# Performance work log

Measured on AMD Instinct MI355X. Metric: run time of the kernel, lower is better.

## Reference

```python
import jax, jax.numpy as jnp
import numpy as np

B, S, D, H = 2, 2048, 2048, 16
DH = D // H  # 128


def _rope_tables(seq_len, head_dim, base=10000.0):
    inv_freq = 1.0 / (base ** (jnp.arange(0, head_dim, 2, dtype=jnp.float32) / head_dim))
    t = jnp.arange(seq_len, dtype=jnp.float32)
    freqs = jnp.outer(t, inv_freq)                      # [S, DH/2]
    emb = jnp.concatenate([freqs, freqs], axis=-1)      # [S, DH]
    return jnp.cos(emb), jnp.sin(emb)


def _rotate_half(x):
    x1, x2 = jnp.split(x, 2, axis=-1)
    return jnp.concatenate([-x2, x1], axis=-1)


def setup_inputs() -> dict:
    key = jax.random.key(0)
    ks = jax.random.split(key, 5)
    sc = 0.02
    return {
        "hidden_states": jax.random.normal(ks[0], (B, S, D), jnp.float32),
        "Wq": jax.random.normal(ks[1], (D, D), jnp.float32) * sc,
        "Wk": jax.random.normal(ks[2], (D, D), jnp.float32) * sc,
        "Wv": jax.random.normal(ks[3], (D, D), jnp.float32) * sc,
        "Wo": jax.random.normal(ks[4], (D, D), jnp.float32) * sc,
        "medical_bias": jnp.zeros((1, H, 1, 1), jnp.float32),
    }


def reference(hidden_states, Wq, Wk, Wv, Wo, medical_bias):
    b, s, _ = hidden_states.shape
    # torch Linear: y = x @ W.T  (W is [out, in])
    def proj(x, W):
        y = jnp.einsum('bsd,ed->bse', x, W)
        return y.reshape(b, s, H, DH).transpose(0, 2, 1, 3)  # [b,H,s,DH]

    q = proj(hidden_states, Wq)
    k = proj(hidden_states, Wk)
    v = proj(hidden_states, Wv)

    cos, sin = _rope_tables(s, DH)                 # [s, DH]
    cos = cos[None, None]                          # [1,1,s,DH]
    sin = sin[None, None]
    q = q * cos + _rotate_half(q) * sin
    k = k * cos + _rotate_half(k) * sin

    scores = jnp.einsum('bhqd,bhkd->bhqk', q, k) / jnp.sqrt(jnp.float32(DH))
    scores = scores + medical_bias                 # learned per-head bias
    probs = jax.nn.softmax(scores, axis=-1)
    out = jnp.einsum('bhqk,bhkd->bhqd', probs, v)  # [b,H,s,DH]
    out = out.transpose(0, 2, 1, 3).reshape(b, s, D)
    return jnp.einsum('bsd,ed->bse', out, Wo)
```

## Files before the change

kernel.cpp:

```cpp
#include <hip/hip_runtime.h>
#include <hip/hip_bf16.h>
#include <stdint.h>


#define B_ 2
#define S_ 2048
#define D_ 2048
#define H_ 16

typedef float f32x4 __attribute__((ext_vector_type(4)));
typedef short s16x8 __attribute__((ext_vector_type(8)));

__device__ __forceinline__ unsigned short f2bf(float f) {
  union { float f; uint32_t u; } c; c.f = f;
  return (unsigned short)((c.u + 0x7fffu + ((c.u >> 16) & 1u)) >> 16);
}

__device__ __forceinline__ unsigned short bfc(float f) {
  __hip_bfloat16 h = __float2bfloat16(f);
  unsigned short u;
  __builtin_memcpy(&u, &h, 2);
  return u;
}

#define FAST_EXP2(x) __builtin_amdgcn_exp2f(x)

__device__ __forceinline__ void gld_lds16(const void* g, void* l) {
  __builtin_amdgcn_global_load_lds(
      (const __attribute__((address_space(1))) uint32_t*)g,
      (__attribute__((address_space(3))) uint32_t*)l, 16, 0, 0);
}

__global__ __launch_bounds__(256) void k_f2bf_all(
    const float* __restrict__ hs, const float* __restrict__ wq,
    const float* __restrict__ wk, const float* __restrict__ wv,
    const float* __restrict__ wo, unsigned short* __restrict__ hb,
    unsigned short* __restrict__ wall, float2* __restrict__ t2) {
  const int NH = 2097152, NW = 1048576;
  const int NF = NH + 4 * NW;
  const int NT = 131072;
  int i = blockIdx.x * 256 + threadIdx.x;
  const int stride = gridDim.x * 256;
  for (; i < NF + NT; i += stride) {
    if (i < NF) {
      f32x4 v;
      ushort4* dst;
      if (i < NH) {
        v = ((const f32x4*)hs)[i];
        dst = (ushort4*)hb + i;
      } else {
        const int j = i - NH;
        const int rgn = j >> 20;
        const int o = j & (NW - 1);
        const float* s = (rgn == 0) ? wq : (rgn == 1) ? wk : (rgn == 2) ? wv : wo;
        v = ((const f32x4*)s)[o];
        dst = (ushort4*)wall + j;
      }
      ushort4 u;
      u.x = f2bf(v.x); u.y = f2bf(v.y); u.z = f2bf(v.z); u.w = f2bf(v.w);
      *dst = u;
    } else {
      const int t = i - NF;
      const int s = t >> 6, j = t & 63;
      float inv = expf(-(float)j * (1.0f / 64.0f) * 9.210340371976184f);
      float sv, cv;
      sincosf((float)s * inv, &sv, &cv);
      t2[t] = float2{cv, sv};
    }
  }
}

__global__ __launch_bounds__(256, 2) void k_gemm(
    const unsigned short* __restrict__ A,
    const unsigned short* __restrict__ W0,
    const unsigned short* __restrict__ W1,
    const unsigned short* __restrict__ W2,
    float* __restrict__ C0,
    unsigned short* __restrict__ Qo,
    unsigned short* __restrict__ Ko,
    unsigned short* __restrict__ VT,
    const float2* __restrict__ tab,
    int plain) {
  __shared__ unsigned short Al[2][128 * 64];
  __shared__ unsigned short Bl[2][128 * 64];

  const int l0 = ((int)blockIdx.z * 32 + (int)blockIdx.y) * 16 + (int)blockIdx.x;
  const int qx = ((int)gridDim.z * 512) >> 3;
  const int wg = (l0 & 7) * qx + (l0 >> 3);
  const int z = wg >> 9;
  const unsigned short* __restrict__ Wp = (z == 0) ? W0 : (z == 1) ? W1 : W2;

  const int tid = threadIdx.x;
  const int w = tid >> 6;
  const int l = tid & 63;
  const int row0 = ((wg >> 4) & 31) * 128;
  const int col0 = (wg & 15) * 128;

  const int c16 = l & 15, g = l >> 4;
  const int cx = c16 & 7;

  const int srow = l >> 3;
  const int sslot = (l & 7) ^ (l >> 3);
  const int scol = sslot << 3;

  int kbase[2];
#pragma unroll
  for (int kk = 0; kk < 2; ++kk)
    kbase[kk] = c16 * 128 + (((kk * 4 + g) ^ cx) << 4);
  const char* AW0 = (const char*)&Al[0][0] + w * 4096;
  const char* AW1 = (const char*)&Al[1][0] + w * 4096;
  const char* BB0 = (const char*)&Bl[0][0];
  const char* BB1 = (const char*)&Bl[1][0];

  f32x4 acc[2][8];
#pragma unroll
  for (int m = 0; m < 2; ++m)
#pragma unroll
    for (int n = 0; n < 8; ++n)
      acc[m][n] = f32x4{0.f, 0.f, 0.f, 0.f};

#define STAGE_G(K0, BUF)                                                       \
  do {                                                                         \
    _Pragma("unroll") for (int i = 0; i < 4; ++i) {                            \
      const int jj = (w << 2) + i;                                             \
      gld_lds16(&A[(size_t)(row0 + (jj << 3) + srow) * 2048 + (K0) + scol],    \
                &Al[BUF][jj * 512]);                                           \
      gld_lds16(&Wp[(size_t)(col0 + (jj << 3) + srow) * 2048 + (K0) + scol],   \
                &Bl[BUF][jj * 512]);                                           \
    }                                                                          \
  } while (0)

#define COMPUTE_G(AW, BBp)                                                     \
  do {                                                                         \
    _Pragma("unroll") for (int kk = 0; kk < 2; ++kk) {                         \
      s16x8 a[2], b[8];                                                        \
      _Pragma("unroll") for (int m = 0; m < 2; ++m)                            \
          a[m] = *(const s16x8*)((AW) + m * 2048 + kbase[kk]);                 \
      _Pragma("unroll") for (int n = 0; n < 8; ++n)                            \
          b[n] = *(const s16x8*)((BBp) + n * 2048 + kbase[kk]);                \
      __builtin_amdgcn_s_setprio(1);                                           \
      _Pragma("unroll") for (int m = 0; m < 2; ++m)                            \
          _Pragma("unroll") for (int n = 0; n < 8; ++n)                        \
              acc[m][n] = __builtin_amdgcn_mfma_f32_16x16x32_bf16(             \
                  a[m], b[n], acc[m][n], 0, 0, 0);                             \
      __builtin_amdgcn_s_setprio(0);                                           \
    }                                                                          \
  } while (0)

  STAGE_G(0, 0);
  __syncthreads();
  for (int k0 = 0; k0 < 2048; k0 += 128) {
    STAGE_G(k0 + 64, 1);
    COMPUTE_G(AW0, BB0);
    __syncthreads();
    if (k0 + 128 < 2048) STAGE_G(k0 + 128, 0);
    COMPUTE_G(AW1, BB1);
    __syncthreads();
  }
#undef STAGE_G
#undef COMPUTE_G

  if (plain) {
#pragma unroll
    for (int m = 0; m < 2; ++m) {
      const int gr = row0 + w * 32 + m * 16 + g * 4;
#pragma unroll
      for (int n = 0; n < 8; ++n) {
        const int gc = col0 + n * 16 + c16;
#pragma unroll
        for (int r = 0; r < 4; ++r)
          C0[(size_t)(gr + r) * 2048 + gc] = acc[m][n][r];
      }
    }
  } else if (z == 2) {
#pragma unroll
    for (int m = 0; m < 2; ++m) {
      const int gr = row0 + w * 32 + m * 16 + g * 4;
      const int b_ = gr >> 11, s_ = gr & 2047;
#pragma unroll
      for (int n = 0; n < 8; ++n) {
        const int gc = col0 + n * 16 + c16;
        ushort4 o;
        o.x = f2bf(acc[m][n][0]);
        o.y = f2bf(acc[m][n][1]);
        o.z = f2bf(acc[m][n][2]);
        o.w = f2bf(acc[m][n][3]);
        *(ushort4*)&VT[((size_t)(b_ * 2048 + gc)) * 2048 + s_] = o;
      }
    }
  } else {
    unsigned short* __restrict__ O = z ? Ko : Qo;
    const float sc = z ? 1.0f : (0.08838834764831845f * 1.4426950408889634f);
#pragma unroll
    for (int m = 0; m < 2; ++m) {
#pragma unroll
      for (int r = 0; r < 4; ++r) {
        const int gr = row0 + w * 32 + m * 16 + g * 4 + r;
        const int s_ = gr & 2047;
#pragma unroll
        for (int n = 0; n < 4; ++n) {
          const float2 f = tab[s_ * 64 + n * 16 + c16];
          const float x1 = acc[m][n][r], x2 = acc[m][n + 4][r];
          O[(size_t)gr * 2048 + col0 + n * 16 + c16] =
              f2bf((x1 * f.x - x2 * f.y) * sc);
          O[(size_t)gr * 2048 + col0 + 64 + n * 16 + c16] =
              f2bf((x2 * f.x + x1 * f.y) * sc);
        }
      }
    }
  }
}

__global__ __launch_bounds__(256, 2) void k_attn(
    const unsigned short* __restrict__ Qb,
    const unsigned short* __restrict__ Kb,
    const unsigned short* __restrict__ Vt,
    unsigned short* __restrict__ Ob) {
  __shared__ unsigned short Kl[2][64 * 128];
  __shared__ unsigned short Vl[2][128 * 64];
  __shared__ unsigned short Pl[4][16 * 64];

  const int l0 = (int)blockIdx.y * 16 + (int)blockIdx.x;
  const int wg = (l0 & 7) * 64 + (l0 >> 3);
  const int bh = wg >> 4;
  const int b = bh >> 4, h = bh & 15;

  const int tid = threadIdx.x, w = tid >> 6, l = tid & 63;
  const int q0 = (wg & 15) * 128 + w * 32;
  const int g = l >> 4, c16 = l & 15;
  const int cx = c16 & 7;

  int kaddr[4], vaddr[2];
#pragma unroll
  for (int kc = 0; kc < 4; ++kc)
    kaddr[kc] = c16 * 256 + ((((kc * 4 + g) ^ cx)) << 4);
#pragma unroll
  for (int kc2 = 0; kc2 < 2; ++kc2)
    vaddr[kc2] = c16 * 128 + ((((kc2 * 4 + g) ^ cx)) << 4);
  const char* PW = (const char*)&Pl[w][0];

  s16x8 qf[2][4];
#pragma unroll
  for (int qq = 0; qq < 2; ++qq)
#pragma unroll
    for (int kc = 0; kc < 4; ++kc)
      qf[qq][kc] = *(const s16x8*)&Qb[(size_t)(b * 2048 + q0 + qq * 16 + c16) * 2048 +
                                      h * 128 + kc * 32 + g * 8];

  f32x4 oacc[2][8];
  float mrow[2][4], lrow[2][4];
#pragma unroll
  for (int qq = 0; qq < 2; ++qq) {
#pragma unroll
    for (int df = 0; df < 8; ++df) oacc[qq][df] = f32x4{0.f, 0.f, 0.f, 0.f};
#pragma unroll
    for (int r = 0; r < 4; ++r) { mrow[qq][r] = -INFINITY; lrow[qq][r] = 0.f; }
  }

#define STAGE(T, BUF)                                                          \
  do {                                                                         \
    _Pragma("unroll") for (int i = 0; i < 4; ++i) {                            \
      const int jj = (w << 2) + i;                                             \
      const int krow = jj * 4 + (l >> 4);                                      \
      const int kslot = (l & 15) ^ (krow & 7);                                 \
      gld_lds16(&Kb[(size_t)(b * 2048 + (T) + krow) * 2048 + h * 128 +        \
                    (kslot << 3)],                                             \
                &Kl[BUF][jj * 512]);                                           \
      const int vrow = jj * 8 + (l >> 3);                                      \
      const int vslot = (l & 7) ^ (vrow & 7);                                  \
      gld_lds16(&Vt[(size_t)(bh * 128 + vrow) * 2048 + (T) + (vslot << 3)],    \
                &Vl[BUF][jj * 512]);                                           \
    }                                                                          \
  } while (0)

#define COMPUTE(BUF_)                                                          \
  do {                                                                         \
    f32x4 sacc[2][4];                                                          \
    _Pragma("unroll") for (int qq = 0; qq < 2; ++qq)                           \
        _Pragma("unroll") for (int n = 0; n < 4; ++n)                          \
            sacc[qq][n] = f32x4{0.f, 0.f, 0.f, 0.f};                           \
    const char* KB = (const char*)&Kl[BUF_][0];                                \
    __builtin_amdgcn_s_setprio(1);                                             \
    _Pragma("unroll") for (int kc = 0; kc < 4; ++kc) {                         \
      s16x8 kb[4];                                                             \
      _Pragma("unroll") for (int n = 0; n < 4; ++n)                            \
          kb[n] = *(const s16x8*)(KB + kaddr[kc] + n * 4096);                  \
      _Pragma("unroll") for (int qq = 0; qq < 2; ++qq)                         \
          _Pragma("unroll") for (int n = 0; n < 4; ++n)                        \
              sacc[qq][n] = __builtin_amdgcn_mfma_f32_16x16x32_bf16(           \
                  qf[qq][kc], kb[n], sacc[qq][n], 0, 0, 0);                    \
    }                                                                          \
    __builtin_amdgcn_s_setprio(0);                                             \
            \
    float mx4[2][4];                                                           \
    float need = 0.f;                                                          \
    _Pragma("unroll") for (int qq = 0; qq < 2; ++qq)                           \
        _Pragma("unroll") for (int r = 0; r < 4; ++r) {                        \
      mx4[qq][r] = fmaxf(fmaxf(sacc[qq][0][r], sacc[qq][1][r]),                \
                         fmaxf(sacc[qq][2][r], sacc[qq][3][r]));               \
      need = fmaxf(need, mx4[qq][r] - mrow[qq][r]);                            \
    }                                                                          \
    if (!__all(need <= 8.0f)) {          \
      _Pragma("unroll") for (int qq = 0; qq < 2; ++qq)                         \
          _Pragma("unroll") for (int r = 0; r < 4; ++r) {                      \
        float mx = mx4[qq][r];                                                 \
        mx = fmaxf(mx, __shfl_xor(mx, 1));                                     \
        mx = fmaxf(mx, __shfl_xor(mx, 2));                                     \
        mx = fmaxf(mx, __shfl_xor(mx, 4));                                     \
        mx = fmaxf(mx, __shfl_xor(mx, 8));                                     \
        float mnew = fmaxf(mrow[qq][r], mx);                                   \
        float alpha = FAST_EXP2(mrow[qq][r] - mnew);                           \
        mrow[qq][r] = mnew;                                                    \
        lrow[qq][r] *= alpha;                                                  \
        _Pragma("unroll") for (int df = 0; df < 8; ++df)                       \
            oacc[qq][df][r] *= alpha;                                          \
      }                                                                        \
    }                                                                          \
    const char* VB = (const char*)&Vl[BUF_][0];                                \
       \
      \
    _Pragma("unroll") for (int qq = 0; qq < 2; ++qq) {                         \
      _Pragma("unroll") for (int r = 0; r < 4; ++r) {                          \
        float rs = 0.f;                                                        \
        _Pragma("unroll") for (int n = 0; n < 4; ++n) {                        \
          float p = FAST_EXP2(sacc[qq][n][r] - mrow[qq][r]);                   \
          sacc[qq][n][r] = p;                                                  \
          rs += p;                                                             \
        }                                                                      \
        lrow[qq][r] += rs;                                                     \
      }                                                                        \
      _Pragma("unroll") for (int n = 0; n < 4; ++n)                            \
          _Pragma("unroll") for (int r = 0; r < 4; ++r) {                      \
        const int prow = g * 4 + r;                                            \
        const int psl = (n * 2 + (c16 >> 3)) ^ (prow & 7);                     \
        Pl[w][prow * 64 + (psl << 3) + (c16 & 7)] = bfc(sacc[qq][n][r]);       \
      }                                                                        \
      __builtin_amdgcn_s_setprio(1);                                           \
      _Pragma("unroll") for (int kc2 = 0; kc2 < 2; ++kc2) {                    \
        s16x8 pa = *(const s16x8*)(PW + vaddr[kc2]);                           \
        _Pragma("unroll") for (int df = 0; df < 8; ++df) {                     \
          s16x8 vb = *(const s16x8*)(VB + vaddr[kc2] + df * 2048);             \
          oacc[qq][df] = __builtin_amdgcn_mfma_f32_16x16x32_bf16(              \
              pa, vb, oacc[qq][df], 0, 0, 0);                                  \
        }                                                                      \
      }                                                                        \
      __builtin_amdgcn_s_setprio(0);                                           \
    }                                                                          \
  } while (0)

  STAGE(0, 0);
  __syncthreads();
  for (int t = 0; t < 2048; t += 128) {
    STAGE(t + 64, 1);
    COMPUTE(0);
    __syncthreads();
    if (t + 128 < 2048) STAGE(t + 128, 0);
    COMPUTE(1);
    __syncthreads();
  }
#undef STAGE
#undef COMPUTE

#pragma unroll
  for (int qq = 0; qq < 2; ++qq)
#pragma unroll
    for (int r = 0; r < 4; ++r) {
      float tot = lrow[qq][r];
      tot += __shfl_xor(tot, 1);
      tot += __shfl_xor(tot, 2);
      tot += __shfl_xor(tot, 4);
      tot += __shfl_xor(tot, 8);
      const float inv = 1.0f / tot;
      const int srow_ = q0 + qq * 16 + g * 4 + r;
#pragma unroll
      for (int df = 0; df < 8; ++df)
        Ob[(size_t)(b * 2048 + srow_) * 2048 + h * 128 + df * 16 + c16] =
            bfc(oacc[qq][df][r] * inv);
    }
}

extern "C" void kernel_launch(void* const* d_in, const int* in_sizes, int n_in,
                              void* d_out, int out_size, void* d_ws, size_t ws_size,
                              hipStream_t stream) {
  const float* hs = (const float*)d_in[0];
  const float* Wq = (const float*)d_in[1];
  const float* Wk = (const float*)d_in[2];
  const float* Wv = (const float*)d_in[3];
  const float* Wo = (const float*)d_in[4];
  float* out = (float*)d_out;
  char* ws = (char*)d_ws;

  unsigned short* hb   = (unsigned short*)(ws + 0);
  unsigned short* wall = (unsigned short*)(ws + 16777216);
  unsigned short* wqb  = wall;
  unsigned short* wkb  = wall + 4194304;
  unsigned short* wvb  = wall + 8388608;
  unsigned short* wob  = wall + 12582912;
  unsigned short* Qbb  = (unsigned short*)(ws + 50331648);
  unsigned short* Kbb  = (unsigned short*)(ws + 67108864);
  unsigned short* Vt   = (unsigned short*)(ws + 83886080);
  float2*         tab2 = (float2*)(ws + 100663296);
  unsigned short* Ob   = hb;

  k_f2bf_all<<<2048, 256, 0, stream>>>(hs, Wq, Wk, Wv, Wo, hb, wall, tab2);

  k_gemm<<<dim3(16, 32, 3), 256, 0, stream>>>(hb, wqb, wkb, wvb, nullptr, Qbb,
                                              Kbb, Vt, tab2, 0);
  k_attn<<<dim3(16, 32), 256, 0, stream>>>(Qbb, Kbb, Vt, Ob);
  k_gemm<<<dim3(16, 32, 1), 256, 0, stream>>>(Ob, wob, nullptr, nullptr, out,
                                              nullptr, nullptr, nullptr, tab2, 1);
}
```

Baseline: 254.1 us.

## Use 256x256 tiles with 512 threads for fused QKV projection GEMM

Adds a dedicated QKV GEMM kernel with 256x256 output tiles, 8 waves, and 128KB of LDS double buffering. Loads are synchronised with explicit vmcnt waits and raw barriers, which gives more operand reuse per loaded byte than the 128x128 tiles. The RoPE epilogue now stages accumulators through LDS so each thread writes coalesced rows. The output projection keeps the original kernel with the mode branches removed. Occupancy drops to one large block per CU, and the grid shrinks to 384 blocks, which may cause tail or load-balance effects.

```diff
diff --git a/kernel.cpp b/kernel.cpp
--- a/kernel.cpp
+++ b/kernel.cpp
@@ -70,25 +70,164 @@
   }
 }
 
-__global__ __launch_bounds__(256, 2) void k_gemm(
+__global__ __launch_bounds__(512, 1) void k_gemm3(
     const unsigned short* __restrict__ A,
     const unsigned short* __restrict__ W0,
     const unsigned short* __restrict__ W1,
     const unsigned short* __restrict__ W2,
-    float* __restrict__ C0,
     unsigned short* __restrict__ Qo,
     unsigned short* __restrict__ Ko,
     unsigned short* __restrict__ VT,
-    const float2* __restrict__ tab,
-    int plain) {
+    const float2* __restrict__ tab) {
+  __shared__ unsigned short Sm[65536];
+
+  const int l0 = ((int)blockIdx.z * 16 + (int)blockIdx.y) * 8 + (int)blockIdx.x;
+  const int wg = (l0 & 7) * 48 + (l0 >> 3);
+  const int z = wg >> 7;
+  const int ww = wg & 127;
+  const int row0 = (ww >> 3) * 256;
+  const int col0 = (ww & 7) * 256;
+  const unsigned short* __restrict__ Wp = (z == 0) ? W0 : (z == 1) ? W1 : W2;
+
+  const int tid = threadIdx.x;
+  const int w = tid >> 6, l = tid & 63;
+  const int wr = w >> 2, wc = w & 3;
+  const int c16 = l & 15, g = l >> 4;
+  const int cx = c16 & 7;
+
+  const int srow = w * 8 + (l >> 3);
+  int kbase[2];
+#pragma unroll
+  for (int kk = 0; kk < 2; ++kk)
+    kbase[kk] = c16 * 128 + (((kk * 4 + g) ^ cx) << 4);
+
+  char* smb = (char*)Sm;
+  const char* AB0 = smb + wr * 16384;
+  const char* AB1 = smb + 32768 + wr * 16384;
+  const char* BB0 = smb + 65536 + wc * 8192;
+  const char* BB1 = smb + 98304 + wc * 8192;
+
+  f32x4 acc[8][4];
+#pragma unroll
+  for (int m = 0; m < 8; ++m)
+#pragma unroll
+    for (int n = 0; n < 4; ++n)
+      acc[m][n] = f32x4{0.f, 0.f, 0.f, 0.f};
+
+#define STAGE3(K0, BUF)                                                        \
+  do {                                                                         \
+    _Pragma("unroll") for (int i = 0; i < 4; ++i) {                            \
+      const int rr = i * 64 + srow;                                            \
+      const int sl = (l & 7) ^ (rr & 7);                                       \
+      gld_lds16(&A[(size_t)(row0 + rr) * 2048 + (K0) + sl * 8],                \
+                Sm + (BUF)*16384 + (i * 64 + w * 8) * 64);                     \
+      gld_lds16(&Wp[(size_t)(col0 + rr) * 2048 + (K0) + sl * 8],               \
+                Sm + 32768 + (BUF)*16384 + (i * 64 + w * 8) * 64);             \
+    }                                                                          \
+  } while (0)
+
+#define COMPUTE3(AB, BB)                                                       \
+  do {                                                                         \
+    _Pragma("unroll") for (int kk = 0; kk < 2; ++kk) {                         \
+      s16x8 a[8], b[4];                                                        \
+      _Pragma("unroll") for (int m = 0; m < 8; ++m)                            \
+          a[m] = *(const s16x8*)((AB) + m * 2048 + kbase[kk]);                 \
+      _Pragma("unroll") for (int n = 0; n < 4; ++n)                            \
+          b[n] = *(const s16x8*)((BB) + n * 2048 + kbase[kk]);                 \
+      __builtin_amdgcn_s_setprio(1);                                           \
+      _Pragma("unroll") for (int m = 0; m < 8; ++m)                            \
+          _Pragma("unroll") for (int n = 0; n < 4; ++n)                        \
+              acc[m][n] = __builtin_amdgcn_mfma_f32_16x16x32_bf16(             \
+                  a[m], b[n], acc[m][n], 0, 0, 0);                             \
+      __builtin_amdgcn_s_setprio(0);                                           \
+    }                                                                          \
+  } while (0)
+
+  STAGE3(0, 0);
+  asm volatile("s_waitcnt vmcnt(0)" ::: "memory");
+  __builtin_amdgcn_s_barrier();
+  for (int k0 = 0; k0 < 2048; k0 += 128) {
+    STAGE3(k0 + 64, 1);
+    asm volatile("s_waitcnt vmcnt(8)" ::: "memory");
+    __builtin_amdgcn_s_barrier();
+    COMPUTE3(AB0, BB0);
+    __builtin_amdgcn_s_barrier();
+    if (k0 + 128 < 2048) {
+      STAGE3(k0 + 128, 0);
+      asm volatile("s_waitcnt vmcnt(8)" ::: "memory");
+    } else {
+      asm volatile("s_waitcnt vmcnt(0)" ::: "memory");
+    }
+    __builtin_amdgcn_s_barrier();
+    COMPUTE3(AB1, BB1);
+    __builtin_amdgcn_s_barrier();
+  }
+#undef STAGE3
+#undef COMPUTE3
+
+  if (z == 2) {
+#pragma unroll
+    for (int m = 0; m < 8; ++m) {
+      const int gr = row0 + wr * 128 + m * 16 + g * 4;
+      const int b_ = gr >> 11, s_ = gr & 2047;
+#pragma unroll
+      for (int n = 0; n < 4; ++n) {
+        const int gc = col0 + wc * 64 + n * 16 + c16;
+        ushort4 o;
+        o.x = bfc(acc[m][n][0]);
+        o.y = bfc(acc[m][n][1]);
+        o.z = bfc(acc[m][n][2]);
+        o.w = bfc(acc[m][n][3]);
+        *(ushort4*)&VT[((size_t)(b_ * 2048 + gc)) * 2048 + s_] = o;
+      }
+    }
+  } else {
+    unsigned short* __restrict__ O = z ? Ko : Qo;
+    const float sc = z ? 1.0f : (0.08838834764831845f * 1.4426950408889634f);
+    float* Ls = (float*)Sm;
+    const int j = tid & 63, rb = tid >> 6;
+#pragma unroll
+    for (int p = 0; p < 2; ++p) {
+      __builtin_amdgcn_s_barrier();
+      if ((wc >> 1) == p) {
+        const int cl0 = (wc & 1) * 64;
+#pragma unroll
+        for (int m = 0; m < 8; ++m)
+#pragma unroll
+          for (int n = 0; n < 4; ++n)
+#pragma unroll
+            for (int r = 0; r < 4; ++r) {
+              const int row = wr * 128 + m * 16 + g * 4 + r;
+              const int col = cl0 + n * 16 + c16;
+              Ls[row * 128 + (col ^ ((row & 4) << 2))] = acc[m][n][r];
+            }
+      }
+      __builtin_amdgcn_s_barrier();
+      const int hc0 = col0 + p * 128;
+#pragma unroll 4
+      for (int i = 0; i < 32; ++i) {
+        const int row = rb + i * 8;
+        const float x1 = Ls[row * 128 + (j ^ ((row & 4) << 2))];
+        const float x2 = Ls[row * 128 + ((j + 64) ^ ((row & 4) << 2))];
+        const int gr = row0 + row;
+        const int s_ = gr & 2047;
+        const float2 f = tab[s_ * 64 + j];
+        O[(size_t)gr * 2048 + hc0 + j] = bfc((x1 * f.x - x2 * f.y) * sc);
+        O[(size_t)gr * 2048 + hc0 + 64 + j] = bfc((x2 * f.x + x1 * f.y) * sc);
+      }
+    }
+  }
+}
+
+__global__ __launch_bounds__(256, 2) void k_gemm(
+    const unsigned short* __restrict__ A,
+    const unsigned short* __restrict__ W0,
+    float* __restrict__ C0) {
   __shared__ unsigned short Al[2][128 * 64];
   __shared__ unsigned short Bl[2][128 * 64];
 
-  const int l0 = ((int)blockIdx.z * 32 + (int)blockIdx.y) * 16 + (int)blockIdx.x;
-  const int qx = ((int)gridDim.z * 512) >> 3;
-  const int wg = (l0 & 7) * qx + (l0 >> 3);
-  const int z = wg >> 9;
-  const unsigned short* __restrict__ Wp = (z == 0) ? W0 : (z == 1) ? W1 : W2;
+  const int l0 = (int)blockIdx.y * 16 + (int)blockIdx.x;
+  const int wg = (l0 & 7) * 64 + (l0 >> 3);
 
   const int tid = threadIdx.x;
   const int w = tid >> 6;
@@ -100,8 +239,7 @@
   const int cx = c16 & 7;
 
   const int srow = l >> 3;
-  const int sslot = (l & 7) ^ (l >> 3);
-  const int scol = sslot << 3;
+  const int scol = ((l & 7) ^ (l >> 3)) << 3;
 
   int kbase[2];
 #pragma unroll
@@ -125,7 +263,7 @@
       const int jj = (w << 2) + i;                                             \
       gld_lds16(&A[(size_t)(row0 + (jj << 3) + srow) * 2048 + (K0) + scol],    \
                 &Al[BUF][jj * 512]);                                           \
-      gld_lds16(&Wp[(size_t)(col0 + (jj << 3) + srow) * 2048 + (K0) + scol],   \
+      gld_lds16(&W0[(size_t)(col0 + (jj << 3) + srow) * 2048 + (K0) + scol],   \
                 &Bl[BUF][jj * 512]);                                           \
     }                                                                          \
   } while (0)
@@ -160,53 +298,15 @@
 #undef STAGE_G
 #undef COMPUTE_G
 
-  if (plain) {
-#pragma unroll
-    for (int m = 0; m < 2; ++m) {
-      const int gr = row0 + w * 32 + m * 16 + g * 4;
-#pragma unroll
-      for (int n = 0; n < 8; ++n) {
-        const int gc = col0 + n * 16 + c16;
-#pragma unroll
-        for (int r = 0; r < 4; ++r)
-          C0[(size_t)(gr + r) * 2048 + gc] = acc[m][n][r];
-      }
-    }
-  } else if (z == 2) {
-#pragma unroll
-    for (int m = 0; m < 2; ++m) {
-      const int gr = row0 + w * 32 + m * 16 + g * 4;
-      const int b_ = gr >> 11, s_ = gr & 2047;
-#pragma unroll
-      for (int n = 0; n < 8; ++n) {
-        const int gc = col0 + n * 16 + c16;
-        ushort4 o;
-        o.x = f2bf(acc[m][n][0]);
-        o.y = f2bf(acc[m][n][1]);
-        o.z = f2bf(acc[m][n][2]);
-        o.w = f2bf(acc[m][n][3]);
-        *(ushort4*)&VT[((size_t)(b_ * 2048 + gc)) * 2048 + s_] = o;
-      }
-    }
-  } else {
-    unsigned short* __restrict__ O = z ? Ko : Qo;
-    const float sc = z ? 1.0f : (0.08838834764831845f * 1.4426950408889634f);
-#pragma unroll
-    for (int m = 0; m < 2; ++m) {
-#pragma unroll
-      for (int r = 0; r < 4; ++r) {
-        const int gr = row0 + w * 32 + m * 16 + g * 4 + r;
-        const int s_ = gr & 2047;
-#pragma unroll
-        for (int n = 0; n < 4; ++n) {
-          const float2 f = tab[s_ * 64 + n * 16 + c16];
-          const float x1 = acc[m][n][r], x2 = acc[m][n + 4][r];
-          O[(size_t)gr * 2048 + col0 + n * 16 + c16] =
-              f2bf((x1 * f.x - x2 * f.y) * sc);
-          O[(size_t)gr * 2048 + col0 + 64 + n * 16 + c16] =
-              f2bf((x2 * f.x + x1 * f.y) * sc);
-        }
-      }
+#pragma unroll
+  for (int m = 0; m < 2; ++m) {
+    const int gr = row0 + w * 32 + m * 16 + g * 4;
+#pragma unroll
+    for (int n = 0; n < 8; ++n) {
+      const int gc = col0 + n * 16 + c16;
+#pragma unroll
+      for (int r = 0; r < 4; ++r)
+        C0[(size_t)(gr + r) * 2048 + gc] = acc[m][n][r];
     }
   }
 }
@@ -291,7 +391,6 @@
                   qf[qq][kc], kb[n], sacc[qq][n], 0, 0, 0);                    \
     }                                                                          \
     __builtin_amdgcn_s_setprio(0);                                             \
-            \
     float mx4[2][4];                                                           \
     float need = 0.f;                                                          \
     _Pragma("unroll") for (int qq = 0; qq < 2; ++qq)                           \
@@ -300,7 +399,7 @@
                          fmaxf(sacc[qq][2][r], sacc[qq][3][r]));               \
       need = fmaxf(need, mx4[qq][r] - mrow[qq][r]);                            \
     }                                                                          \
-    if (!__all(need <= 8.0f)) {          \
+    if (!__all(need <= 8.0f)) {                                                \
       _Pragma("unroll") for (int qq = 0; qq < 2; ++qq)                         \
           _Pragma("unroll") for (int r = 0; r < 4; ++r) {                      \
         float mx = mx4[qq][r];                                                 \
@@ -317,8 +416,6 @@
       }                                                                        \
     }                                                                          \
     const char* VB = (const char*)&Vl[BUF_][0];                                \
-       \
-      \
     _Pragma("unroll") for (int qq = 0; qq < 2; ++qq) {                         \
       _Pragma("unroll") for (int r = 0; r < 4; ++r) {                          \
         float rs = 0.f;                                                        \
@@ -404,9 +501,8 @@
 
   k_f2bf_all<<<2048, 256, 0, stream>>>(hs, Wq, Wk, Wv, Wo, hb, wall, tab2);
 
-  k_gemm<<<dim3(16, 32, 3), 256, 0, stream>>>(hb, wqb, wkb, wvb, nullptr, Qbb,
-                                              Kbb, Vt, tab2, 0);
+  k_gemm3<<<dim3(8, 16, 3), 512, 0, stream>>>(hb, wqb, wkb, wvb, Qbb, Kbb, Vt,
+                                              tab2);
   k_attn<<<dim3(16, 32), 256, 0, stream>>>(Qbb, Kbb, Vt, Ob);
-  k_gemm<<<dim3(16, 32, 1), 256, 0, stream>>>(Ob, wob, nullptr, nullptr, out,
-                                              nullptr, nullptr, nullptr, tab2, 1);
-}
+  k_gemm<<<dim3(16, 32), 256, 0, stream>>>(Ob, wob, out);
+}
```

Result: slower. 366.5 us (+44.2%).

## Split QKV projection into dedicated kernel with 256x128 tiles and triple-buffered pipeline

Applied to the files above, without the earlier changes.

Adds a dedicated QKV projection kernel that uses 256x128 output tiles (4x8 MFMA accumulators per wave) with a K-step of 32. Loads are triple-buffered and overlapped with compute through explicit vmcnt waits and raw barriers in place of __syncthreads. The aim is more operand reuse per loaded byte and better overlap of global loads with compute. The output GEMM keeps the old kernel with the dead branches removed. The larger accumulator set raises register pressure and halves the block count, which can hurt occupancy or leave the grid poorly balanced.

```diff
diff --git a/kernel.cpp b/kernel.cpp
--- a/kernel.cpp
+++ b/kernel.cpp
@@ -70,25 +70,139 @@
   }
 }
 
-__global__ __launch_bounds__(256, 2) void k_gemm(
+__global__ __launch_bounds__(256, 2) void k_gemmq(
     const unsigned short* __restrict__ A,
     const unsigned short* __restrict__ W0,
     const unsigned short* __restrict__ W1,
     const unsigned short* __restrict__ W2,
-    float* __restrict__ C0,
     unsigned short* __restrict__ Qo,
     unsigned short* __restrict__ Ko,
     unsigned short* __restrict__ VT,
-    const float2* __restrict__ tab,
-    int plain) {
+    const float2* __restrict__ tab) {
+  __shared__ unsigned short Al[3][256 * 32];
+  __shared__ unsigned short Bl[3][128 * 32];
+
+  const int l0 = ((int)blockIdx.z * 16 + (int)blockIdx.y) * 16 + (int)blockIdx.x;
+  const int wg = (l0 & 7) * 96 + (l0 >> 3);
+  const int z = wg >> 8;
+  const int ww = wg & 255;
+  const int row0 = (ww >> 4) * 256;
+  const int col0 = (ww & 15) * 128;
+  const unsigned short* __restrict__ Wp = (z == 0) ? W0 : (z == 1) ? W1 : W2;
+
+  const int tid = threadIdx.x;
+  const int w = tid >> 6, l = tid & 63;
+  const int c16 = l & 15, g = l >> 4;
+
+  const int sr = w * 16 + (l >> 2);
+  const int ssl = (l & 3) ^ ((l >> 3) & 3);
+  const int scol = ssl << 3;
+
+  const int swz = g ^ ((c16 >> 1) & 3);
+  const int abase = (w * 64 + c16) * 64 + swz * 16;
+  const int bbase = c16 * 64 + swz * 16;
+
+  f32x4 acc[4][8];
+#pragma unroll
+  for (int m = 0; m < 4; ++m)
+#pragma unroll
+    for (int n = 0; n < 8; ++n)
+      acc[m][n] = f32x4{0.f, 0.f, 0.f, 0.f};
+
+#define STAGE_Q(K0, BUF)                                                       \
+  do {                                                                         \
+    _Pragma("unroll") for (int i = 0; i < 4; ++i)                              \
+        gld_lds16(&A[(size_t)(row0 + i * 64 + sr) * 2048 + (K0) + scol],       \
+                  &Al[BUF][(i * 64 + w * 16) * 32]);                           \
+    _Pragma("unroll") for (int j = 0; j < 2; ++j)                              \
+        gld_lds16(&Wp[(size_t)(col0 + j * 64 + sr) * 2048 + (K0) + scol],      \
+                  &Bl[BUF][(j * 64 + w * 16) * 32]);                           \
+  } while (0)
+
+#define COMPUTE_Q(BUF)                                                         \
+  do {                                                                         \
+    const char* AB = (const char*)&Al[0][0] + (BUF)*16384;                     \
+    const char* BB = (const char*)&Bl[0][0] + (BUF)*8192;                      \
+    s16x8 a[4], b[8];                                                          \
+    _Pragma("unroll") for (int m = 0; m < 4; ++m)                              \
+        a[m] = *(const s16x8*)(AB + abase + m * 1024);                         \
+    _Pragma("unroll") for (int n = 0; n < 8; ++n)                              \
+        b[n] = *(const s16x8*)(BB + bbase + n * 1024);                         \
+    __builtin_amdgcn_s_setprio(1);                                             \
+    _Pragma("unroll") for (int m = 0; m < 4; ++m)                              \
+        _Pragma("unroll") for (int n = 0; n < 8; ++n)                          \
+            acc[m][n] = __builtin_amdgcn_mfma_f32_16x16x32_bf16(               \
+                a[m], b[n], acc[m][n], 0, 0, 0);                               \
+    __builtin_amdgcn_s_setprio(0);                                             \
+  } while (0)
+
+  STAGE_Q(0, 0);
+  STAGE_Q(32, 1);
+  int bcur = 0, bnxt = 2;
+  for (int t = 0; t < 64; ++t) {
+    if (t < 62) {
+      STAGE_Q((t + 2) * 32, bnxt);
+      asm volatile("s_waitcnt vmcnt(6)" ::: "memory");
+    } else {
+      asm volatile("s_waitcnt vmcnt(0)" ::: "memory");
+    }
+    asm volatile("s_barrier" ::: "memory");
+    COMPUTE_Q(bcur);
+    asm volatile("s_barrier" ::: "memory");
+    bcur = (bcur == 2) ? 0 : bcur + 1;
+    bnxt = (bnxt == 2) ? 0 : bnxt + 1;
+  }
+#undef STAGE_Q
+#undef COMPUTE_Q
+
+  if (z == 2) {
+#pragma unroll
+    for (int m = 0; m < 4; ++m) {
+      const int gr = row0 + w * 64 + m * 16 + g * 4;
+      const int b_ = gr >> 11, s_ = gr & 2047;
+#pragma unroll
+      for (int n = 0; n < 8; ++n) {
+        const int gc = col0 + n * 16 + c16;
+        ushort4 o;
+        o.x = bfc(acc[m][n][0]);
+        o.y = bfc(acc[m][n][1]);
+        o.z = bfc(acc[m][n][2]);
+        o.w = bfc(acc[m][n][3]);
+        *(ushort4*)&VT[((size_t)(b_ * 2048 + gc)) * 2048 + s_] = o;
+      }
+    }
+  } else {
+    unsigned short* __restrict__ O = z ? Ko : Qo;
+    const float sc = z ? 1.0f : (0.08838834764831845f * 1.4426950408889634f);
+#pragma unroll
+    for (int m = 0; m < 4; ++m) {
+#pragma unroll
+      for (int r = 0; r < 4; ++r) {
+        const int gr = row0 + w * 64 + m * 16 + g * 4 + r;
+        const int s_ = gr & 2047;
+#pragma unroll
+        for (int n = 0; n < 4; ++n) {
+          const float2 f = tab[s_ * 64 + n * 16 + c16];
+          const float x1 = acc[m][n][r], x2 = acc[m][n + 4][r];
+          O[(size_t)gr * 2048 + col0 + n * 16 + c16] =
+              bfc((x1 * f.x - x2 * f.y) * sc);
+          O[(size_t)gr * 2048 + col0 + 64 + n * 16 + c16] =
+              bfc((x2 * f.x + x1 * f.y) * sc);
+        }
+      }
+    }
+  }
+}
+
+__global__ __launch_bounds__(256, 2) void k_gemm(
+    const unsigned short* __restrict__ A,
+    const unsigned short* __restrict__ W0,
+    float* __restrict__ C0) {
   __shared__ unsigned short Al[2][128 * 64];
   __shared__ unsigned short Bl[2][128 * 64];
 
-  const int l0 = ((int)blockIdx.z * 32 + (int)blockIdx.y) * 16 + (int)blockIdx.x;
-  const int qx = ((int)gridDim.z * 512) >> 3;
-  const int wg = (l0 & 7) * qx + (l0 >> 3);
-  const int z = wg >> 9;
-  const unsigned short* __restrict__ Wp = (z == 0) ? W0 : (z == 1) ? W1 : W2;
+  const int l0 = (int)blockIdx.y * 16 + (int)blockIdx.x;
+  const int wg = (l0 & 7) * 64 + (l0 >> 3);
 
   const int tid = threadIdx.x;
   const int w = tid >> 6;
@@ -100,8 +214,7 @@
   const int cx = c16 & 7;
 
   const int srow = l >> 3;
-  const int sslot = (l & 7) ^ (l >> 3);
-  const int scol = sslot << 3;
+  const int scol = ((l & 7) ^ (l >> 3)) << 3;
 
   int kbase[2];
 #pragma unroll
@@ -125,7 +238,7 @@
       const int jj = (w << 2) + i;                                             \
       gld_lds16(&A[(size_t)(row0 + (jj << 3) + srow) * 2048 + (K0) + scol],    \
                 &Al[BUF][jj * 512]);                                           \
-      gld_lds16(&Wp[(size_t)(col0 + (jj << 3) + srow) * 2048 + (K0) + scol],   \
+      gld_lds16(&W0[(size_t)(col0 + (jj << 3) + srow) * 2048 + (K0) + scol],   \
                 &Bl[BUF][jj * 512]);                                           \
     }                                                                          \
   } while (0)
@@ -160,53 +273,15 @@
 #undef STAGE_G
 #undef COMPUTE_G
 
-  if (plain) {
-#pragma unroll
-    for (int m = 0; m < 2; ++m) {
-      const int gr = row0 + w * 32 + m * 16 + g * 4;
-#pragma unroll
-      for (int n = 0; n < 8; ++n) {
-        const int gc = col0 + n * 16 + c16;
-#pragma unroll
-        for (int r = 0; r < 4; ++r)
-          C0[(size_t)(gr + r) * 2048 + gc] = acc[m][n][r];
-      }
-    }
-  } else if (z == 2) {
-#pragma unroll
-    for (int m = 0; m < 2; ++m) {
-      const int gr = row0 + w * 32 + m * 16 + g * 4;
-      const int b_ = gr >> 11, s_ = gr & 2047;
-#pragma unroll
-      for (int n = 0; n < 8; ++n) {
-        const int gc = col0 + n * 16 + c16;
-        ushort4 o;
-        o.x = f2bf(acc[m][n][0]);
-        o.y = f2bf(acc[m][n][1]);
-        o.z = f2bf(acc[m][n][2]);
-        o.w = f2bf(acc[m][n][3]);
-        *(ushort4*)&VT[((size_t)(b_ * 2048 + gc)) * 2048 + s_] = o;
-      }
-    }
-  } else {
-    unsigned short* __restrict__ O = z ? Ko : Qo;
-    const float sc = z ? 1.0f : (0.08838834764831845f * 1.4426950408889634f);
-#pragma unroll
-    for (int m = 0; m < 2; ++m) {
-#pragma unroll
-      for (int r = 0; r < 4; ++r) {
-        const int gr = row0 + w * 32 + m * 16 + g * 4 + r;
-        const int s_ = gr & 2047;
-#pragma unroll
-        for (int n = 0; n < 4; ++n) {
-          const float2 f = tab[s_ * 64 + n * 16 + c16];
-          const float x1 = acc[m][n][r], x2 = acc[m][n + 4][r];
-          O[(size_t)gr * 2048 + col0 + n * 16 + c16] =
-              f2bf((x1 * f.x - x2 * f.y) * sc);
-          O[(size_t)gr * 2048 + col0 + 64 + n * 16 + c16] =
-              f2bf((x2 * f.x + x1 * f.y) * sc);
-        }
-      }
+#pragma unroll
+  for (int m = 0; m < 2; ++m) {
+    const int gr = row0 + w * 32 + m * 16 + g * 4;
+#pragma unroll
+    for (int n = 0; n < 8; ++n) {
+      const int gc = col0 + n * 16 + c16;
+#pragma unroll
+      for (int r = 0; r < 4; ++r)
+        C0[(size_t)(gr + r) * 2048 + gc] = acc[m][n][r];
     }
   }
 }
@@ -291,7 +366,6 @@
                   qf[qq][kc], kb[n], sacc[qq][n], 0, 0, 0);                    \
     }                                                                          \
     __builtin_amdgcn_s_setprio(0);                                             \
-            \
     float mx4[2][4];                                                           \
     float need = 0.f;                                                          \
     _Pragma("unroll") for (int qq = 0; qq < 2; ++qq)                           \
@@ -317,8 +391,6 @@
       }                                                                        \
     }                                                                          \
     const char* VB = (const char*)&Vl[BUF_][0];                                \
-       \
-      \
     _Pragma("unroll") for (int qq = 0; qq < 2; ++qq) {                         \
       _Pragma("unroll") for (int r = 0; r < 4; ++r) {                          \
         float rs = 0.f;                                                        \
@@ -404,9 +476,8 @@
 
   k_f2bf_all<<<2048, 256, 0, stream>>>(hs, Wq, Wk, Wv, Wo, hb, wall, tab2);
 
-  k_gemm<<<dim3(16, 32, 3), 256, 0, stream>>>(hb, wqb, wkb, wvb, nullptr, Qbb,
-                                              Kbb, Vt, tab2, 0);
+  k_gemmq<<<dim3(16, 16, 3), 256, 0, stream>>>(hb, wqb, wkb, wvb, Qbb, Kbb, Vt,
+                                               tab2);
   k_attn<<<dim3(16, 32), 256, 0, stream>>>(Qbb, Kbb, Vt, Ob);
-  k_gemm<<<dim3(16, 32, 1), 256, 0, stream>>>(Ob, wob, nullptr, nullptr, out,
-                                              nullptr, nullptr, nullptr, tab2, 1);
-}
+  k_gemm<<<dim3(16, 32), 256, 0, stream>>>(Ob, wob, out);
+}
```

Measured after the change: 280.6 us. 10.4% more time.
